# Kernel tuning notes

Hardware: AMD Instinct MI355X
Metric: run time of the kernel (lower is better)

The kernel has to match this reference:

```python
import jax, jax.numpy as jnp
import numpy as np
from itertools import product


def _gen_exps(num_vars, degree):
    return [e for e in product(range(degree + 1), repeat=num_vars) if sum(e) <= degree]

EXP_W = _gen_exps(7, 3)  # 120 terms
EXP_B = _gen_exps(3, 3)  # 20 terms
EXP_M = _gen_exps(5, 3)  # 56 terms (+1 diagonal coeff)


def _powers(x, exps):
    return {e: x ** e for e in exps}


def setup_inputs() -> dict:
    key = jax.random.key(0)
    ks = jax.random.split(key, 12)
    B, Din, Dout = 65536, 64, 64
    return {
        'x1': jax.random.normal(ks[0], (B, Din), jnp.float32),
        's1': jax.random.normal(ks[1], (B, Dout), jnp.float32),
        'y1': jax.random.normal(ks[2], (B, Dout), jnp.float32),
        'x2': jax.random.normal(ks[3], (B, Din), jnp.float32),
        's2': jax.random.normal(ks[4], (B, Dout), jnp.float32),
        'y2': jax.random.normal(ks[5], (B, Dout), jnp.float32),
        'w': jax.random.normal(ks[6], (Dout, Din), jnp.float32) * 0.1,
        'b': jax.random.normal(ks[7], (Dout,), jnp.float32) * 0.1,
        'm': jax.random.normal(ks[8], (Dout, Dout), jnp.float32) * 0.1,
        'params_w': jax.random.normal(ks[9], (len(EXP_W),), jnp.float32) * 0.1,
        'params_b': jax.random.normal(ks[10], (len(EXP_B),), jnp.float32) * 0.1,
        'params_m': jax.random.normal(ks[11], (len(EXP_M) + 1,), jnp.float32) * 0.1,
    }


def _dw(x1, s1, y1, x2, s2, y2, w, params_w):
    px1 = _powers(x1, {e[0] for e in EXP_W})
    ps1 = _powers(s1, {e[1] for e in EXP_W})
    py1 = _powers(y1, {e[2] for e in EXP_W})
    px2 = _powers(x2, {e[3] for e in EXP_W})
    ps2 = _powers(s2, {e[4] for e in EXP_W})
    py2 = _powers(y2, {e[5] for e in EXP_W})
    pw = _powers(w, {e[6] for e in EXP_W})
    inv_b = 1.0 / x1.shape[0]
    delta_w = jnp.zeros_like(w)
    for i, e in enumerate(EXP_W):
        y_term = ps1[e[1]] * py1[e[2]] * ps2[e[4]] * py2[e[5]]  # [B, Dout]
        x_term = px1[e[0]] * px2[e[3]]                          # [B, Din]
        delta_w = delta_w + (params_w[i] * inv_b) * (y_term.T @ x_term) * pw[e[6]]
    return delta_w  # bound=None (identity), l2_reg=0


def _db(y1, y2, b, params_b):
    py1 = _powers(y1, {e[0] for e in EXP_B})
    py2 = _powers(y2, {e[1] for e in EXP_B})
    pb = _powers(b, {e[2] for e in EXP_B})
    inv_b = 1.0 / y1.shape[0]
    delta_b = jnp.zeros_like(b)
    for i, e in enumerate(EXP_B):
        delta_b = delta_b + (params_b[i] * inv_b) * jnp.sum(py1[e[0]] * py2[e[1]], axis=0) * pb[e[2]]
    return delta_b


def _dm(y1, y2, m, params_m):
    ey1 = {e[0] for e in EXP_M} | {e[1] for e in EXP_M}
    ey2 = {e[2] for e in EXP_M} | {e[3] for e in EXP_M}
    py1 = _powers(y1, ey1)
    py2 = _powers(y2, ey2)
    pm = _powers(m, {e[4] for e in EXP_M})
    inv_b = 1.0 / y1.shape[0]
    delta_m = jnp.zeros_like(m)
    for i, e in enumerate(EXP_M):
        left = py1[e[1]] * py2[e[3]]   # [B, Dout]
        right = py1[e[0]] * py2[e[2]]  # [B, Dout]
        delta_m = delta_m + (params_m[i] * inv_b) * (left.T @ right) * pm[e[4]]
    delta_m = delta_m + params_m[-1] * jnp.eye(m.shape[0], dtype=m.dtype)
    return delta_m


def reference(x1, s1, y1, x2, s2, y2, w, b, m, params_w, params_b, params_m):
    delta_w = _dw(x1, s1, y1, x2, s2, y2, w, params_w)
    delta_b = _db(y1, y2, b, params_b)
    delta_m = _dm(y1, y2, m, params_m)
    return delta_w, delta_b, delta_m
```

## Files before the change

kernel.cpp:

```cpp
#include <hip/hip_runtime.h>
#include <type_traits>
#include <stdint.h>

#define DEV __device__ __forceinline__

typedef float f32x4 __attribute__((ext_vector_type(4)));
typedef short bf16x8 __attribute__((ext_vector_type(8)));
typedef unsigned short u16;
typedef u16 u16x8 __attribute__((ext_vector_type(8)));

static constexpr int BTOT = 65536;
static constexpr int KB   = 64;
static constexpr int NCHT = BTOT / KB;
static constexpr int NG   = 56;
static constexpr int NCOLSUM = 45;
static constexpr float INVB = 1.0f / (float)BTOT;

static constexpr int NWIN  = 32;
static constexpr int CHW   = NCHT / NWIN;
static constexpr int NCOLG = 7;
static constexpr int GRID  = 8*NWIN;
static constexpr int BUFHALF = 8*4096;

struct Col {
  int nslot, np;
  int8_t sexp[8][6];
  int8_t pa[8], pb[8];
  int16_t gout[8];
  uint8_t ldmask;
};

struct Tables {
  int nW, nB, nM, nA, nX;
  int8_t expw[120][7];
  int8_t expb[20][3];
  int8_t expm[56][5];
  int8_t am[35][4];
  int8_t xm[10][2];
  Col col[NCOLG];
  int8_t wtype[120]; int16_t widx[120]; int8_t wpow[120];
  int8_t mtype[56];  int16_t midx[56];  int8_t mpow[56];
  int16_t bcol[20];  int8_t bpow[20];
  int err, gcount;
};

constexpr int aidf(const Tables& t,int a,int b,int c,int d){
  for(int i=0;i<t.nA;i++)
    if(t.am[i][0]==a&&t.am[i][1]==b&&t.am[i][2]==c&&t.am[i][3]==d) return i;
  return -1;
}
constexpr int xidf(const Tables& t,int a,int b){
  for(int i=0;i<t.nX;i++) if(t.xm[i][0]==a&&t.xm[i][1]==b) return i;
  return -1;
}

constexpr Tables makeTables(){
  Tables t{};
  t.err = 0;
  t.nW=0;
  for(int e0=0;e0<4;e0++)for(int e1=0;e1<4;e1++)for(int e2=0;e2<4;e2++)
  for(int e3=0;e3<4;e3++)for(int e4=0;e4<4;e4++)for(int e5=0;e5<4;e5++)
  for(int e6=0;e6<4;e6++) if(e0+e1+e2+e3+e4+e5+e6<=3){
    t.expw[t.nW][0]=(int8_t)e0; t.expw[t.nW][1]=(int8_t)e1; t.expw[t.nW][2]=(int8_t)e2;
    t.expw[t.nW][3]=(int8_t)e3; t.expw[t.nW][4]=(int8_t)e4; t.expw[t.nW][5]=(int8_t)e5;
    t.expw[t.nW][6]=(int8_t)e6; t.nW++;
  }
  t.nB=0;
  for(int e0=0;e0<4;e0++)for(int e1=0;e1<4;e1++)for(int e2=0;e2<4;e2++)
    if(e0+e1+e2<=3){ t.expb[t.nB][0]=(int8_t)e0; t.expb[t.nB][1]=(int8_t)e1; t.expb[t.nB][2]=(int8_t)e2; t.nB++; }
  t.nM=0;
  for(int e0=0;e0<4;e0++)for(int e1=0;e1<4;e1++)for(int e2=0;e2<4;e2++)
  for(int e3=0;e3<4;e3++)for(int e4=0;e4<4;e4++)
    if(e0+e1+e2+e3+e4<=3){
      t.expm[t.nM][0]=(int8_t)e0; t.expm[t.nM][1]=(int8_t)e1; t.expm[t.nM][2]=(int8_t)e2;
      t.expm[t.nM][3]=(int8_t)e3; t.expm[t.nM][4]=(int8_t)e4; t.nM++;
    }
  t.nA=0;
  for(int a=0;a<4;a++)for(int b=0;b<4;b++)for(int c=0;c<4;c++)for(int d=0;d<4;d++)
    if(a+b+c+d<=3){ t.am[t.nA][0]=(int8_t)a; t.am[t.nA][1]=(int8_t)b; t.am[t.nA][2]=(int8_t)c; t.am[t.nA][3]=(int8_t)d; t.nA++; }
  t.nX=0;
  for(int a=0;a<4;a++)for(int b=0;b<4;b++)
    if(a+b<=3){ t.xm[t.nX][0]=(int8_t)a; t.xm[t.nX][1]=(int8_t)b; t.nX++; }

  int wslot[35][10]; int mslot[10][10];
  for(int i=0;i<35;i++)for(int j=0;j<10;j++) wslot[i][j]=-1;
  for(int i=0;i<10;i++)for(int j=0;j<10;j++) mslot[i][j]=-1;

  int slot=0;

  {
    Col& c=t.col[0]; c.nslot=4; c.np=8;
    int ym[4][2]={{0,1},{1,0},{0,2},{1,1}};
    for(int s=0;s<4;s++){ for(int q=0;q<6;q++)c.sexp[s][q]=0;
      c.sexp[s][1]=(int8_t)ym[s][0]; c.sexp[s][3]=(int8_t)ym[s][1]; }
    int p=0;
    for(int L=0;L<2;L++)for(int R=0;R<4;R++){
      c.pa[p]=(int8_t)L; c.pb[p]=(int8_t)R; c.gout[p]=(int16_t)slot;
      mslot[xidf(t,ym[L][0],ym[L][1])][xidf(t,ym[R][0],ym[R][1])]=slot; slot++; p++;
    }
  }
  {
    Col& c=t.col[1]; c.nslot=5; c.np=8;
    int ym[5][2]={{0,1},{1,0},{0,2},{1,1},{2,0}};
    for(int s=0;s<5;s++){ for(int q=0;q<6;q++)c.sexp[s][q]=0;
      c.sexp[s][1]=(int8_t)ym[s][0]; c.sexp[s][3]=(int8_t)ym[s][1]; }
    int p=0;
    for(int L=0;L<2;L++){
      c.pa[p]=(int8_t)L; c.pb[p]=4; c.gout[p]=(int16_t)slot;
      mslot[xidf(t,ym[L][0],ym[L][1])][xidf(t,2,0)]=slot; slot++; p++;
    }
    for(int i=0;i<3;i++)for(int j=0;j<2;j++){
      c.pa[p]=(int8_t)(2+i); c.pb[p]=(int8_t)j; c.gout[p]=(int16_t)slot;
      mslot[xidf(t,ym[2+i][0],ym[2+i][1])][xidf(t,ym[j][0],ym[j][1])]=slot; slot++; p++;
    }
  }
  for(int wc=0; wc<2; wc++){
    Col& c=t.col[2+2*wc]; c.nslot=6; c.np=8;
    int am2[2][2]={{1,0},{0,1}};
    int xb[4][2]={{0,1},{1,0},{0,2},{1,1}};
    for(int s=0;s<6;s++) for(int q=0;q<6;q++) c.sexp[s][q]=0;
    for(int s=0;s<2;s++){
      c.sexp[s][wc?2:0]=(int8_t)am2[s][0]; c.sexp[s][wc?3:1]=(int8_t)am2[s][1];
    }
    for(int s=0;s<4;s++){ c.sexp[2+s][4]=(int8_t)xb[s][0]; c.sexp[2+s][5]=(int8_t)xb[s][1]; }
    int p=0;
    for(int a=0;a<2;a++)for(int b=0;b<4;b++){
      int amid = wc? aidf(t,0,0,am2[a][0],am2[a][1]) : aidf(t,am2[a][0],am2[a][1],0,0);
      if(amid<0) t.err+=1;
      c.pa[p]=(int8_t)a; c.pb[p]=(int8_t)(2+b); c.gout[p]=(int16_t)slot;
      wslot[amid][xidf(t,xb[b][0],xb[b][1])]=slot; slot++; p++;
    }
  }
  for(int wc=0; wc<2; wc++){
    Col& c=t.col[3+2*wc]; c.nslot=8; c.np=8;
    int am5[5][2]={{1,0},{0,1},{2,0},{1,1},{0,2}};
    int xb[3][2]={{2,0},{0,1},{1,0}};
    for(int s=0;s<8;s++) for(int q=0;q<6;q++) c.sexp[s][q]=0;
    for(int s=0;s<5;s++){
      c.sexp[s][wc?2:0]=(int8_t)am5[s][0]; c.sexp[s][wc?3:1]=(int8_t)am5[s][1];
    }
    for(int s=0;s<3;s++){ c.sexp[5+s][4]=(int8_t)xb[s][0]; c.sexp[5+s][5]=(int8_t)xb[s][1]; }
    int p=0;
    for(int a=0;a<2;a++){
      int amid = wc? aidf(t,0,0,am5[a][0],am5[a][1]) : aidf(t,am5[a][0],am5[a][1],0,0);
      if(amid<0) t.err+=1;
      c.pa[p]=(int8_t)a; c.pb[p]=5; c.gout[p]=(int16_t)slot;
      wslot[amid][xidf(t,2,0)]=slot; slot++; p++;
    }
    for(int i=0;i<3;i++)for(int j=0;j<2;j++){
      int amid = wc? aidf(t,0,0,am5[2+i][0],am5[2+i][1]) : aidf(t,am5[2+i][0],am5[2+i][1],0,0);
      if(amid<0) t.err+=1;
      c.pa[p]=(int8_t)(2+i); c.pb[p]=(int8_t)(6+j); c.gout[p]=(int16_t)slot;
      wslot[amid][xidf(t,xb[1+j][0],xb[1+j][1])]=slot; slot++; p++;
    }
  }
  {
    Col& c=t.col[6]; c.nslot=6; c.np=8;
    int a4[4][4]={{1,0,1,0},{1,0,0,1},{0,1,1,0},{0,1,0,1}};
    int xb[2][2]={{0,1},{1,0}};
    for(int s=0;s<6;s++) for(int q=0;q<6;q++) c.sexp[s][q]=0;
    for(int s=0;s<4;s++) for(int q=0;q<4;q++) c.sexp[s][q]=(int8_t)a4[s][q];
    for(int s=0;s<2;s++){ c.sexp[4+s][4]=(int8_t)xb[s][0]; c.sexp[4+s][5]=(int8_t)xb[s][1]; }
    int p=0;
    for(int a=0;a<4;a++)for(int b=0;b<2;b++){
      int amid = aidf(t,a4[a][0],a4[a][1],a4[a][2],a4[a][3]);
      if(amid<0) t.err+=1;
      c.pa[p]=(int8_t)a; c.pb[p]=(int8_t)(4+b); c.gout[p]=(int16_t)slot;
      wslot[amid][xidf(t,xb[b][0],xb[b][1])]=slot; slot++; p++;
    }
  }
  t.gcount=slot;
  if(slot!=NG) t.err+=1;

  for(int ci=0; ci<NCOLG; ci++){
    unsigned m=0;
    for(int s=0;s<t.col[ci].nslot;s++)
      for(int v=0;v<6;v++) if(t.col[ci].sexp[s][v]>0) m |= (1u<<v);
    t.col[ci].ldmask=(uint8_t)m;
  }

  for(int i=0;i<t.nW;i++){
    const int8_t* e=t.expw[i];
    bool u0=(e[0]==0&&e[3]==0);
    bool v0=(e[1]==0&&e[2]==0&&e[4]==0&&e[5]==0);
    t.wpow[i]=e[6];
    if(u0){ t.wtype[i]=1; t.widx[i]=(int16_t)aidf(t,e[1],e[2],e[4],e[5]); }
    else if(v0){ t.wtype[i]=2; t.widx[i]=(int16_t)xidf(t,e[0],e[3]); }
    else {
      int s=wslot[aidf(t,e[1],e[2],e[4],e[5])][xidf(t,e[0],e[3])];
      if(s<0) t.err+=1;
      t.wtype[i]=0; t.widx[i]=(int16_t)s;
    }
  }
  for(int i=0;i<t.nM;i++){
    const int8_t* e=t.expm[i];
    bool L0=(e[1]==0&&e[3]==0), R0=(e[0]==0&&e[2]==0);
    t.mpow[i]=e[4];
    if(L0){ t.mtype[i]=2; t.midx[i]=(int16_t)aidf(t,0,e[0],0,e[2]); }
    else if(R0){ t.mtype[i]=1; t.midx[i]=(int16_t)aidf(t,0,e[1],0,e[3]); }
    else {
      int s=mslot[xidf(t,e[1],e[3])][xidf(t,e[0],e[2])];
      if(s<0) t.err+=1;
      t.mtype[i]=0; t.midx[i]=(int16_t)s;
    }
  }
  for(int i=0;i<t.nB;i++){
    const int8_t* e=t.expb[i];
    t.bcol[i]=(int16_t)aidf(t,0,e[0],0,e[1]); t.bpow[i]=e[2];
  }
  return t;
}

constexpr Tables TB = makeTables();
static_assert(TB.err==0 && TB.gcount==56, "table build failed");
static_assert(TB.nW==120 && TB.nB==20 && TB.nM==56 && TB.nA==35 && TB.nX==10, "enumeration mismatch");

template<int N, typename F>
DEV void sunroll(F&& f){
  if constexpr (N > 0){
    sunroll<N-1>(static_cast<F&&>(f));
    f(std::integral_constant<int, N-1>{});
  }
}
template<int E> DEV float ipw(float x){
  if constexpr(E==0) return 1.0f;
  else if constexpr(E==1) return x;
  else if constexpr(E==2) return x*x;
  else return x*x*x;
}
DEV u16 f2bf(float f){
  uint32_t u = __builtin_bit_cast(uint32_t, f);
  u = u + 0x7FFFu + ((u>>16)&1u);
  return (u16)(u>>16);
}

DEV bf16x8 readFrag(const u16* L, int slot, int sb, int tt, int l){
  return *(const bf16x8*)&L[slot*4096 + ((sb*4 + tt)*64 + l)*8];
}
DEV f32x4 mfma_(bf16x8 a, bf16x8 b, f32x4 c){
  return __builtin_amdgcn_mfma_f32_16x16x32_bf16(a, b, c, 0, 0, 0);
}

template<int CI>
DEV void colGemm(const float* __restrict__ s1,const float* __restrict__ y1,
                 const float* __restrict__ s2,const float* __restrict__ y2,
                 const float* __restrict__ x1,const float* __restrict__ x2,
                 float* __restrict__ G, u16* lds, int tid, int bi)
{
  constexpr int NS = TB.col[CI].nslot;
  constexpr unsigned LM = TB.col[CI].ldmask;

  const int l = tid&63, w = tid>>6;
  const int c0 = bi*CHW, c1 = c0+CHW;

  if (w < 8){
    const int pw = w;
    const int wrbase = ((pw>>2)*4 + (l>>4))*512 + ((pw&3)*16 + (l&15))*8;
    float rw[6][8];

    auto LOAD = [&](int ck){
      const int b0 = (ck*KB + pw*8)*64 + l;
      #pragma unroll
      for(int j=0;j<8;j++){
        const int off = b0 + j*64;
        if constexpr(LM&1u)  rw[0][j]=s1[off];
        if constexpr(LM&2u)  rw[1][j]=y1[off];
        if constexpr(LM&4u)  rw[2][j]=s2[off];
        if constexpr(LM&8u)  rw[3][j]=y2[off];
        if constexpr(LM&16u) rw[4][j]=x1[off];
        if constexpr(LM&32u) rw[5][j]=x2[off];
      }
    };
    auto PROD = [&](int buf){
      u16* L = lds + buf*BUFHALF;
      sunroll<NS>([&](auto S){
        constexpr int s = decltype(S)::value;
        u16x8 o8;
        #pragma unroll
        for(int j=0;j<8;j++){
          float v = ipw<TB.col[CI].sexp[s][0]>(rw[0][j])
                  * ipw<TB.col[CI].sexp[s][1]>(rw[1][j])
                  * ipw<TB.col[CI].sexp[s][2]>(rw[2][j])
                  * ipw<TB.col[CI].sexp[s][3]>(rw[3][j])
                  * ipw<TB.col[CI].sexp[s][4]>(rw[4][j])
                  * ipw<TB.col[CI].sexp[s][5]>(rw[5][j]);
          o8[j]=f2bf(v);
        }
        *(u16x8*)&L[s*4096 + wrbase] = o8;
      });
    };

    LOAD(c0); PROD(c0&1);
    asm volatile("s_waitcnt lgkmcnt(0)" ::: "memory");
    __builtin_amdgcn_s_barrier();
    __builtin_amdgcn_sched_barrier(0);

    for(int k=c0; k<c1; ++k){
      if(k+1 < c1){ LOAD(k+1); PROD((k+1)&1); }
      asm volatile("s_waitcnt lgkmcnt(0)" ::: "memory");
      __builtin_amdgcn_s_barrier();
      __builtin_amdgcn_sched_barrier(0);
    }
  } else {
    int aslot=0, bslot=0, gsl=0;
    sunroll<8>([&](auto PP){
      constexpr int p = decltype(PP)::value;
      if(w == 8+p){
        aslot = TB.col[CI].pa[p];
        bslot = TB.col[CI].pb[p];
        gsl   = TB.col[CI].gout[p];
      }
    });
    f32x4 acc[4][4] = {};

    __builtin_amdgcn_s_barrier();
    __builtin_amdgcn_sched_barrier(0);

    for(int k=c0; k<c1; ++k){
      const u16* L = lds + (k&1)*BUFHALF;
      __builtin_amdgcn_s_setprio(1);
      #pragma unroll
      for(int sb=0; sb<2; ++sb){
        bf16x8 Af[4];
        #pragma unroll
        for(int o2=0;o2<4;o2++) Af[o2]=readFrag(L,aslot,sb,o2,l);
        #pragma unroll
        for(int dd=0;dd<4;dd++){
          bf16x8 Bf=readFrag(L,bslot,sb,dd,l);
          #pragma unroll
          for(int o2=0;o2<4;o2++) acc[o2][dd]=mfma_(Af[o2],Bf,acc[o2][dd]);
        }
      }
      __builtin_amdgcn_s_setprio(0);
      asm volatile("s_waitcnt lgkmcnt(0)" ::: "memory");
      __builtin_amdgcn_s_barrier();
      __builtin_amdgcn_sched_barrier(0);
    }

    const int r0=(l>>4)*4, cc=l&15;
    float* dst = G + gsl*4096;
    #pragma unroll
    for(int o2=0;o2<4;o2++)
      #pragma unroll
      for(int dd=0;dd<4;dd++)
        #pragma unroll
        for(int r=0;r<4;r++)
          atomicAdd(&dst[(o2*16+r0+r)*64 + dd*16+cc], acc[o2][dd][r]);
  }
}

DEV void colRed(const float* __restrict__ s1,const float* __restrict__ y1,
                const float* __restrict__ s2,const float* __restrict__ y2,
                const float* __restrict__ x1,const float* __restrict__ x2,
                float* __restrict__ col, float* ldsF, int tid, int bi)
{
  const int ch=tid&63, g16=tid>>6;
  const int base = bi*2048;
  float accv[45];
  sunroll<45>([&](auto K){ accv[decltype(K)::value]=0.f; });
  for(int r=base+g16; r<base+2048; r+=16){
    const int off=r*64+ch;
    const float v0=s1[off],v1=y1[off],v2=s2[off],v3=y2[off],v4=x1[off],v5=x2[off];
    sunroll<35>([&](auto K){
      constexpr int k=decltype(K)::value;
      accv[k] += ipw<TB.am[k][0]>(v0)*ipw<TB.am[k][1]>(v1)*ipw<TB.am[k][2]>(v2)*ipw<TB.am[k][3]>(v3);
    });
    sunroll<10>([&](auto K){
      constexpr int k=decltype(K)::value;
      accv[35+k] += ipw<TB.xm[k][0]>(v4)*ipw<TB.xm[k][1]>(v5);
    });
  }
  sunroll<6>([&](auto RR){
    constexpr int rr=decltype(RR)::value;
    __syncthreads();
    sunroll<8>([&](auto Q){
      constexpr int q=decltype(Q)::value;
      if constexpr(rr*8+q < 45)
        ldsF[(q*16+g16)*64+ch]=accv[rr*8+q];
    });
    __syncthreads();
    {
      const int k=tid>>6, c=tid&63;
      const int idx=rr*8+k;
      if(k<8 && idx<45){
        float s=0.f;
        #pragma unroll
        for(int gg=0; gg<16; gg++) s+=ldsF[(k*16+gg)*64+c];
        atomicAdd(&col[idx*64+c], s);
      }
    }
  });
}

__global__ __launch_bounds__(1024, 4) void k_main(
    const float* __restrict__ x1, const float* __restrict__ s1, const float* __restrict__ y1,
    const float* __restrict__ x2, const float* __restrict__ s2, const float* __restrict__ y2,
    float* __restrict__ G, float* __restrict__ col)
{
  __shared__ u16 lds[2*BUFHALF];
  const int tid = threadIdx.x;
  const int u = blockIdx.x >> 5;
  const int g = blockIdx.x & 31;
  if      (u==0) colGemm<0>(s1,y1,s2,y2,x1,x2,G,lds,tid,g);
  else if (u==1) colGemm<1>(s1,y1,s2,y2,x1,x2,G,lds,tid,g);
  else if (u==2) colGemm<2>(s1,y1,s2,y2,x1,x2,G,lds,tid,g);
  else if (u==3) colGemm<3>(s1,y1,s2,y2,x1,x2,G,lds,tid,g);
  else if (u==4) colGemm<4>(s1,y1,s2,y2,x1,x2,G,lds,tid,g);
  else if (u==5) colGemm<5>(s1,y1,s2,y2,x1,x2,G,lds,tid,g);
  else if (u==6) colGemm<6>(s1,y1,s2,y2,x1,x2,G,lds,tid,g);
  else           colRed(s1,y1,s2,y2,x1,x2,col,(float*)lds,tid,g);
}

__global__ __launch_bounds__(256) void k_combine(
    const float* __restrict__ G, const float* __restrict__ col,
    const float* __restrict__ w, const float* __restrict__ b, const float* __restrict__ m,
    const float* __restrict__ parw, const float* __restrict__ parb, const float* __restrict__ parm,
    float* __restrict__ out)
{
  const int n = blockIdx.x*256 + threadIdx.x;
  const int o = n>>6, d = n&63;
  const float wv = w[n], mv = m[n];
  const float wp[4] = {1.f, wv, wv*wv, wv*wv*wv};
  const float mp[4] = {1.f, mv, mv*mv, mv*mv*mv};
  float aw=0.f, am=0.f;
  sunroll<120>([&](auto II){
    constexpr int i = decltype(II)::value;
    constexpr int ty = TB.wtype[i];
    constexpr int ix = TB.widx[i];
    constexpr int q  = TB.wpow[i];
    float val;
    if constexpr(ty==0) val = G[ix*4096 + n];
    else if constexpr(ty==1) val = col[ix*64 + o];
    else val = col[(35+ix)*64 + d];
    aw += parw[i] * val * wp[q];
  });
  sunroll<56>([&](auto II){
    constexpr int i = decltype(II)::value;
    constexpr int ty = TB.mtype[i];
    constexpr int ix = TB.midx[i];
    constexpr int q  = TB.mpow[i];
    float val;
    if constexpr(ty==0) val = G[ix*4096 + n];
    else if constexpr(ty==1) val = col[ix*64 + o];
    else val = col[ix*64 + d];
    am += parm[i] * val * mp[q];
  });
  aw *= INVB; am *= INVB;
  if (o==d) am += parm[56];
  out[n] = aw;
  out[4160 + n] = am;
  if (n < 64){
    const float bv = b[n];
    const float bp[4] = {1.f, bv, bv*bv, bv*bv*bv};
    float ab=0.f;
    sunroll<20>([&](auto II){
      constexpr int i = decltype(II)::value;
      constexpr int cix = TB.bcol[i];
      constexpr int q = TB.bpow[i];
      ab += parb[i] * col[cix*64 + n] * bp[q];
    });
    out[4096 + n] = ab * INVB;
  }
}

extern "C" void kernel_launch(void* const* d_in, const int* in_sizes, int n_in,
                              void* d_out, int out_size, void* d_ws, size_t ws_size,
                              hipStream_t stream)
{
  const float* x1=(const float*)d_in[0];
  const float* s1=(const float*)d_in[1];
  const float* y1=(const float*)d_in[2];
  const float* x2=(const float*)d_in[3];
  const float* s2=(const float*)d_in[4];
  const float* y2=(const float*)d_in[5];
  const float* w =(const float*)d_in[6];
  const float* b =(const float*)d_in[7];
  const float* m =(const float*)d_in[8];
  const float* parw=(const float*)d_in[9];
  const float* parb=(const float*)d_in[10];
  const float* parm=(const float*)d_in[11];

  float* G   = (float*)d_ws;
  float* col = G + NG*4096;

  hipMemsetAsync(d_ws, 0, (size_t)(NG*4096 + NCOLSUM*64)*sizeof(float), stream);
  k_main<<<GRID, 1024, 0, stream>>>(x1,s1,y1,x2,s2,y2,G,col);
  k_combine<<<16, 256, 0, stream>>>(G,col,w,b,m,parw,parb,parm,(float*)d_out);
}
```

Measured before the change: 107.7 us.

## Fuse column-sum reductions into GEMM producer warps and drop separate reduction blocks

The separate colRed block group, which re-read all six inputs to compute the 45 column sums, is removed. Each column sum is now assigned at compile time to the GEMM column group whose producer warps already load the needed inputs, and is accumulated from the staged registers. The grid shrinks from 8 to 7 block groups, cutting redundant global reads. The change also swaps warp roles (MFMA consumers now in warps 0-7), drops the setprio hint, prefetches input loads one chunk further ahead, and relaxes the launch-bounds occupancy hint, which adds register pressure in the producer warps.

```diff
diff --git a/kernel.cpp b/kernel.cpp
--- a/kernel.cpp
+++ b/kernel.cpp
@@ -19,7 +19,7 @@
 static constexpr int NWIN  = 32;
 static constexpr int CHW   = NCHT / NWIN;
 static constexpr int NCOLG = 7;
-static constexpr int GRID  = 8*NWIN;
+static constexpr int GRID  = NCOLG*NWIN;
 static constexpr int BUFHALF = 8*4096;
 
 struct Col {
@@ -28,6 +28,9 @@
   int8_t pa[8], pb[8];
   int16_t gout[8];
   uint8_t ldmask;
+  int ncs;
+  int8_t csexp[13][6];
+  int8_t csidx[13];
 };
 
 struct Tables {
@@ -41,7 +44,7 @@
   int8_t wtype[120]; int16_t widx[120]; int8_t wpow[120];
   int8_t mtype[56];  int16_t midx[56];  int8_t mpow[56];
   int16_t bcol[20];  int8_t bpow[20];
-  int err, gcount;
+  int err, gcount, cscover;
 };
 
 constexpr int aidf(const Tables& t,int a,int b,int c,int d){
@@ -179,6 +182,34 @@
     t.col[ci].ldmask=(uint8_t)m;
   }
 
+  t.cscover=0;
+  for(int i=0;i<t.nA;i++){
+    const int8_t* e=t.am[i];
+    int target;
+    if(e[0]==0&&e[2]==0) target=0;
+    else if(e[2]==0&&e[3]==0) target=3;
+    else if(e[0]==0&&e[1]==0) target=5;
+    else target=6;
+    Col& c=t.col[target];
+    c.csexp[c.ncs][0]=e[0]; c.csexp[c.ncs][1]=e[1];
+    c.csexp[c.ncs][2]=e[2]; c.csexp[c.ncs][3]=e[3];
+    c.csexp[c.ncs][4]=0; c.csexp[c.ncs][5]=0;
+    c.csidx[c.ncs]=(int8_t)i; c.ncs++; t.cscover++;
+  }
+  for(int i=0;i<t.nX;i++){
+    Col& c=t.col[2];
+    c.csexp[c.ncs][0]=0; c.csexp[c.ncs][1]=0; c.csexp[c.ncs][2]=0; c.csexp[c.ncs][3]=0;
+    c.csexp[c.ncs][4]=t.xm[i][0]; c.csexp[c.ncs][5]=t.xm[i][1];
+    c.csidx[c.ncs]=(int8_t)(35+i); c.ncs++; t.cscover++;
+  }
+  if(t.cscover!=NCOLSUM) t.err+=1;
+  for(int ci=0; ci<NCOLG; ci++){
+    if(t.col[ci].ncs>13) t.err+=1;
+    for(int k=0;k<t.col[ci].ncs;k++)
+      for(int v=0;v<6;v++)
+        if(t.col[ci].csexp[k][v]>0 && !((t.col[ci].ldmask>>v)&1u)) t.err+=1;
+  }
+
   for(int i=0;i<t.nW;i++){
     const int8_t* e=t.expw[i];
     bool u0=(e[0]==0&&e[3]==0);
@@ -212,7 +243,7 @@
 }
 
 constexpr Tables TB = makeTables();
-static_assert(TB.err==0 && TB.gcount==56, "table build failed");
+static_assert(TB.err==0 && TB.gcount==56 && TB.cscover==45, "table build failed");
 static_assert(TB.nW==120 && TB.nB==20 && TB.nM==56 && TB.nA==35 && TB.nX==10, "enumeration mismatch");
 
 template<int N, typename F>
@@ -245,21 +276,68 @@
 DEV void colGemm(const float* __restrict__ s1,const float* __restrict__ y1,
                  const float* __restrict__ s2,const float* __restrict__ y2,
                  const float* __restrict__ x1,const float* __restrict__ x2,
-                 float* __restrict__ G, u16* lds, int tid, int bi)
+                 float* __restrict__ G, float* __restrict__ col,
+                 u16* lds, int tid, int bi)
 {
   constexpr int NS = TB.col[CI].nslot;
+  constexpr int NCS = TB.col[CI].ncs;
   constexpr unsigned LM = TB.col[CI].ldmask;
 
   const int l = tid&63, w = tid>>6;
   const int c0 = bi*CHW, c1 = c0+CHW;
 
   if (w < 8){
-    const int pw = w;
-    const int wrbase = ((pw>>2)*4 + (l>>4))*512 + ((pw&3)*16 + (l&15))*8;
+    int aslot=0, bslot=0, gsl=0;
+    sunroll<8>([&](auto PP){
+      constexpr int p = decltype(PP)::value;
+      if(w == p){
+        aslot = TB.col[CI].pa[p];
+        bslot = TB.col[CI].pb[p];
+        gsl   = TB.col[CI].gout[p];
+      }
+    });
+    f32x4 acc[4][4] = {};
+
+    __builtin_amdgcn_s_barrier();
+    __builtin_amdgcn_sched_barrier(0);
+
+    for(int k=c0; k<c1; ++k){
+      const u16* L = lds + (k&1)*BUFHALF;
+      #pragma unroll
+      for(int sb=0; sb<2; ++sb){
+        bf16x8 Af[4];
+        #pragma unroll
+        for(int o2=0;o2<4;o2++) Af[o2]=readFrag(L,aslot,sb,o2,l);
+        #pragma unroll
+        for(int dd=0;dd<4;dd++){
+          bf16x8 Bf=readFrag(L,bslot,sb,dd,l);
+          #pragma unroll
+          for(int o2=0;o2<4;o2++) acc[o2][dd]=mfma_(Af[o2],Bf,acc[o2][dd]);
+        }
+      }
+      asm volatile("s_waitcnt lgkmcnt(0)" ::: "memory");
+      __builtin_amdgcn_s_barrier();
+      __builtin_amdgcn_sched_barrier(0);
+    }
+
+    const int r0=(l>>4)*4, cc=l&15;
+    float* dst = G + gsl*4096;
+    #pragma unroll
+    for(int o2=0;o2<4;o2++)
+      #pragma unroll
+      for(int dd=0;dd<4;dd++)
+        #pragma unroll
+        for(int r=0;r<4;r++)
+          atomicAdd(&dst[(o2*16+r0+r)*64 + dd*16+cc], acc[o2][dd][r]);
+  } else {
+    const int sw = w-8;
+    const int wrbase = ((sw>>2)*4 + (l>>4))*512 + ((sw&3)*16 + (l&15))*8;
     float rw[6][8];
+    float csum[NCS>0?NCS:1];
+    sunroll<(NCS>0?NCS:1)>([&](auto C){ csum[decltype(C)::value]=0.f; });
 
     auto LOAD = [&](int ck){
-      const int b0 = (ck*KB + pw*8)*64 + l;
+      const int b0 = (ck*KB + sw*8)*64 + l;
       #pragma unroll
       for(int j=0;j<8;j++){
         const int off = b0 + j*64;
@@ -271,7 +349,7 @@
         if constexpr(LM&32u) rw[5][j]=x2[off];
       }
     };
-    auto PROD = [&](int buf){
+    auto STAGE = [&](int buf){
       u16* L = lds + buf*BUFHALF;
       sunroll<NS>([&](auto S){
         constexpr int s = decltype(S)::value;
@@ -289,110 +367,47 @@
         *(u16x8*)&L[s*4096 + wrbase] = o8;
       });
     };
-
-    LOAD(c0); PROD(c0&1);
+    auto CSUM = [&]{
+      sunroll<NCS>([&](auto C){
+        constexpr int c = decltype(C)::value;
+        float s0 = 0.f;
+        #pragma unroll
+        for(int j=0;j<8;j++){
+          s0 += ipw<TB.col[CI].csexp[c][0]>(rw[0][j])
+              * ipw<TB.col[CI].csexp[c][1]>(rw[1][j])
+              * ipw<TB.col[CI].csexp[c][2]>(rw[2][j])
+              * ipw<TB.col[CI].csexp[c][3]>(rw[3][j])
+              * ipw<TB.col[CI].csexp[c][4]>(rw[4][j])
+              * ipw<TB.col[CI].csexp[c][5]>(rw[5][j]);
+        }
+        csum[c] += s0;
+      });
+    };
+
+    LOAD(c0); STAGE(c0&1); CSUM(); LOAD(c0+1);
     asm volatile("s_waitcnt lgkmcnt(0)" ::: "memory");
     __builtin_amdgcn_s_barrier();
     __builtin_amdgcn_sched_barrier(0);
 
     for(int k=c0; k<c1; ++k){
-      if(k+1 < c1){ LOAD(k+1); PROD((k+1)&1); }
+      if(k+1 < c1){
+        STAGE((k+1)&1);
+        CSUM();
+        if(k+2 < c1) LOAD(k+2);
+      }
       asm volatile("s_waitcnt lgkmcnt(0)" ::: "memory");
       __builtin_amdgcn_s_barrier();
       __builtin_amdgcn_sched_barrier(0);
     }
-  } else {
-    int aslot=0, bslot=0, gsl=0;
-    sunroll<8>([&](auto PP){
-      constexpr int p = decltype(PP)::value;
-      if(w == 8+p){
-        aslot = TB.col[CI].pa[p];
-        bslot = TB.col[CI].pb[p];
-        gsl   = TB.col[CI].gout[p];
-      }
+
+    sunroll<NCS>([&](auto C){
+      constexpr int c = decltype(C)::value;
+      atomicAdd(&col[(int)TB.col[CI].csidx[c]*64 + l], csum[c]);
     });
-    f32x4 acc[4][4] = {};
-
-    __builtin_amdgcn_s_barrier();
-    __builtin_amdgcn_sched_barrier(0);
-
-    for(int k=c0; k<c1; ++k){
-      const u16* L = lds + (k&1)*BUFHALF;
-      __builtin_amdgcn_s_setprio(1);
-      #pragma unroll
-      for(int sb=0; sb<2; ++sb){
-        bf16x8 Af[4];
-        #pragma unroll
-        for(int o2=0;o2<4;o2++) Af[o2]=readFrag(L,aslot,sb,o2,l);
-        #pragma unroll
-        for(int dd=0;dd<4;dd++){
-          bf16x8 Bf=readFrag(L,bslot,sb,dd,l);
-          #pragma unroll
-          for(int o2=0;o2<4;o2++) acc[o2][dd]=mfma_(Af[o2],Bf,acc[o2][dd]);
-        }
-      }
-      __builtin_amdgcn_s_setprio(0);
-      asm volatile("s_waitcnt lgkmcnt(0)" ::: "memory");
-      __builtin_amdgcn_s_barrier();
-      __builtin_amdgcn_sched_barrier(0);
-    }
-
-    const int r0=(l>>4)*4, cc=l&15;
-    float* dst = G + gsl*4096;
-    #pragma unroll
-    for(int o2=0;o2<4;o2++)
-      #pragma unroll
-      for(int dd=0;dd<4;dd++)
-        #pragma unroll
-        for(int r=0;r<4;r++)
-          atomicAdd(&dst[(o2*16+r0+r)*64 + dd*16+cc], acc[o2][dd][r]);
-  }
-}
-
-DEV void colRed(const float* __restrict__ s1,const float* __restrict__ y1,
-                const float* __restrict__ s2,const float* __restrict__ y2,
-                const float* __restrict__ x1,const float* __restrict__ x2,
-                float* __restrict__ col, float* ldsF, int tid, int bi)
-{
-  const int ch=tid&63, g16=tid>>6;
-  const int base = bi*2048;
-  float accv[45];
-  sunroll<45>([&](auto K){ accv[decltype(K)::value]=0.f; });
-  for(int r=base+g16; r<base+2048; r+=16){
-    const int off=r*64+ch;
-    const float v0=s1[off],v1=y1[off],v2=s2[off],v3=y2[off],v4=x1[off],v5=x2[off];
-    sunroll<35>([&](auto K){
-      constexpr int k=decltype(K)::value;
-      accv[k] += ipw<TB.am[k][0]>(v0)*ipw<TB.am[k][1]>(v1)*ipw<TB.am[k][2]>(v2)*ipw<TB.am[k][3]>(v3);
-    });
-    sunroll<10>([&](auto K){
-      constexpr int k=decltype(K)::value;
-      accv[35+k] += ipw<TB.xm[k][0]>(v4)*ipw<TB.xm[k][1]>(v5);
-    });
-  }
-  sunroll<6>([&](auto RR){
-    constexpr int rr=decltype(RR)::value;
-    __syncthreads();
-    sunroll<8>([&](auto Q){
-      constexpr int q=decltype(Q)::value;
-      if constexpr(rr*8+q < 45)
-        ldsF[(q*16+g16)*64+ch]=accv[rr*8+q];
-    });
-    __syncthreads();
-    {
-      const int k=tid>>6, c=tid&63;
-      const int idx=rr*8+k;
-      if(k<8 && idx<45){
-        float s=0.f;
-        #pragma unroll
-        for(int gg=0; gg<16; gg++) s+=ldsF[(k*16+gg)*64+c];
-        atomicAdd(&col[idx*64+c], s);
-      }
-    }
-  });
-}
-
-__global__ __launch_bounds__(1024, 4) void k_main(
+  }
+}
+
+__global__ __launch_bounds__(1024) void k_main(
     const float* __restrict__ x1, const float* __restrict__ s1, const float* __restrict__ y1,
     const float* __restrict__ x2, const float* __restrict__ s2, const float* __restrict__ y2,
     float* __restrict__ G, float* __restrict__ col)
@@ -401,14 +416,13 @@
   const int tid = threadIdx.x;
   const int u = blockIdx.x >> 5;
   const int g = blockIdx.x & 31;
-  if      (u==0) colGemm<0>(s1,y1,s2,y2,x1,x2,G,lds,tid,g);
-  else if (u==1) colGemm<1>(s1,y1,s2,y2,x1,x2,G,lds,tid,g);
-  else if (u==2) colGemm<2>(s1,y1,s2,y2,x1,x2,G,lds,tid,g);
-  else if (u==3) colGemm<3>(s1,y1,s2,y2,x1,x2,G,lds,tid,g);
-  else if (u==4) colGemm<4>(s1,y1,s2,y2,x1,x2,G,lds,tid,g);
-  else if (u==5) colGemm<5>(s1,y1,s2,y2,x1,x2,G,lds,tid,g);
-  else if (u==6) colGemm<6>(s1,y1,s2,y2,x1,x2,G,lds,tid,g);
-  else           colRed(s1,y1,s2,y2,x1,x2,col,(float*)lds,tid,g);
+  if      (u==0) colGemm<0>(s1,y1,s2,y2,x1,x2,G,col,lds,tid,g);
+  else if (u==1) colGemm<1>(s1,y1,s2,y2,x1,x2,G,col,lds,tid,g);
+  else if (u==2) colGemm<2>(s1,y1,s2,y2,x1,x2,G,col,lds,tid,g);
+  else if (u==3) colGemm<3>(s1,y1,s2,y2,x1,x2,G,col,lds,tid,g);
+  else if (u==4) colGemm<4>(s1,y1,s2,y2,x1,x2,G,col,lds,tid,g);
+  else if (u==5) colGemm<5>(s1,y1,s2,y2,x1,x2,G,col,lds,tid,g);
+  else           colGemm<6>(s1,y1,s2,y2,x1,x2,G,col,lds,tid,g);
 }
 
 __global__ __launch_bounds__(256) void k_combine(
```

Result: slower. 280.4 us (+160.3%).

## Merge producer and MFMA waves into unified 512-thread blocks with more windows

Applied to the files above, without the earlier changes.

Drops warp specialization, in which 8 waves produced bf16 power products into a double-buffered LDS and 8 other waves ran MFMAs. Now every wave of a 512-thread block computes its own products, writes them to a single LDS buffer, then runs its GEMM slot pair, with two barriers per chunk. The grid doubles to 64 windows per column group, and the column-reduction blocks are adjusted to 8 row groups. This halves LDS use and may let more blocks fit per CU, at the cost of losing the overlap between product computation and MFMA within a block and doubling the atomic adds to G.

```diff
diff --git a/kernel.cpp b/kernel.cpp
--- a/kernel.cpp
+++ b/kernel.cpp
@@ -16,11 +16,10 @@
 static constexpr int NCOLSUM = 45;
 static constexpr float INVB = 1.0f / (float)BTOT;
 
-static constexpr int NWIN  = 32;
+static constexpr int NWIN  = 64;
 static constexpr int CHW   = NCHT / NWIN;
 static constexpr int NCOLG = 7;
 static constexpr int GRID  = 8*NWIN;
-static constexpr int BUFHALF = 8*4096;
 
 struct Col {
   int nslot, np;
@@ -251,102 +250,81 @@
   constexpr unsigned LM = TB.col[CI].ldmask;
 
   const int l = tid&63, w = tid>>6;
+  const int wrbase = ((w>>2)*4 + (l>>4))*512 + ((w&3)*16 + (l&15))*8;
+
+  int aslot=0, bslot=0, gsl=0;
+  sunroll<8>([&](auto PP){
+    constexpr int p = decltype(PP)::value;
+    if(w == p){
+      aslot = TB.col[CI].pa[p];
+      bslot = TB.col[CI].pb[p];
+      gsl   = TB.col[CI].gout[p];
+    }
+  });
+
   const int c0 = bi*CHW, c1 = c0+CHW;
-
-  if (w < 8){
-    const int pw = w;
-    const int wrbase = ((pw>>2)*4 + (l>>4))*512 + ((pw&3)*16 + (l&15))*8;
-    float rw[6][8];
-
-    auto LOAD = [&](int ck){
-      const int b0 = (ck*KB + pw*8)*64 + l;
-      #pragma unroll
-      for(int j=0;j<8;j++){
-        const int off = b0 + j*64;
-        if constexpr(LM&1u)  rw[0][j]=s1[off];
-        if constexpr(LM&2u)  rw[1][j]=y1[off];
-        if constexpr(LM&4u)  rw[2][j]=s2[off];
-        if constexpr(LM&8u)  rw[3][j]=y2[off];
-        if constexpr(LM&16u) rw[4][j]=x1[off];
-        if constexpr(LM&32u) rw[5][j]=x2[off];
-      }
-    };
-    auto PROD = [&](int buf){
-      u16* L = lds + buf*BUFHALF;
+  f32x4 acc[4][4] = {};
+
+  for(int k=c0; k<c1; ++k){
+    u16x8 o8v[NS];
+    const int b0 = (k*KB + w*8)*64 + l;
+    #pragma unroll
+    for(int j=0;j<8;j++){
+      const int off = b0 + j*64;
+      float v0=0,v1=0,v2=0,v3=0,v4=0,v5=0;
+      if constexpr(LM&1u)  v0=s1[off];
+      if constexpr(LM&2u)  v1=y1[off];
+      if constexpr(LM&4u)  v2=s2[off];
+      if constexpr(LM&8u)  v3=y2[off];
+      if constexpr(LM&16u) v4=x1[off];
+      if constexpr(LM&32u) v5=x2[off];
       sunroll<NS>([&](auto S){
         constexpr int s = decltype(S)::value;
-        u16x8 o8;
-        #pragma unroll
-        for(int j=0;j<8;j++){
-          float v = ipw<TB.col[CI].sexp[s][0]>(rw[0][j])
-                  * ipw<TB.col[CI].sexp[s][1]>(rw[1][j])
-                  * ipw<TB.col[CI].sexp[s][2]>(rw[2][j])
-                  * ipw<TB.col[CI].sexp[s][3]>(rw[3][j])
-                  * ipw<TB.col[CI].sexp[s][4]>(rw[4][j])
-                  * ipw<TB.col[CI].sexp[s][5]>(rw[5][j]);
-          o8[j]=f2bf(v);
-        }
-        *(u16x8*)&L[s*4096 + wrbase] = o8;
+        float v = ipw<TB.col[CI].sexp[s][0]>(v0)
+                * ipw<TB.col[CI].sexp[s][1]>(v1)
+                * ipw<TB.col[CI].sexp[s][2]>(v2)
+                * ipw<TB.col[CI].sexp[s][3]>(v3)
+                * ipw<TB.col[CI].sexp[s][4]>(v4)
+                * ipw<TB.col[CI].sexp[s][5]>(v5);
+        o8v[s][j] = f2bf(v);
       });
-    };
-
-    LOAD(c0); PROD(c0&1);
+    }
+    sunroll<NS>([&](auto S){
+      constexpr int s = decltype(S)::value;
+      *(u16x8*)&lds[s*4096 + wrbase] = o8v[s];
+    });
+
     asm volatile("s_waitcnt lgkmcnt(0)" ::: "memory");
     __builtin_amdgcn_s_barrier();
     __builtin_amdgcn_sched_barrier(0);
 
-    for(int k=c0; k<c1; ++k){
-      if(k+1 < c1){ LOAD(k+1); PROD((k+1)&1); }
-      asm volatile("s_waitcnt lgkmcnt(0)" ::: "memory");
-      __builtin_amdgcn_s_barrier();
-      __builtin_amdgcn_sched_barrier(0);
-    }
-  } else {
-    int aslot=0, bslot=0, gsl=0;
-    sunroll<8>([&](auto PP){
-      constexpr int p = decltype(PP)::value;
-      if(w == 8+p){
-        aslot = TB.col[CI].pa[p];
-        bslot = TB.col[CI].pb[p];
-        gsl   = TB.col[CI].gout[p];
+    #pragma unroll
+    for(int sb=0; sb<2; ++sb){
+      bf16x8 Af[4];
+      #pragma unroll
+      for(int o2=0;o2<4;o2++) Af[o2]=readFrag(lds,aslot,sb,o2,l);
+      #pragma unroll
+      for(int dd=0;dd<4;dd++){
+        bf16x8 Bf=readFrag(lds,bslot,sb,dd,l);
+        #pragma unroll
+        for(int o2=0;o2<4;o2++) acc[o2][dd]=mfma_(Af[o2],Bf,acc[o2][dd]);
       }
-    });
-    f32x4 acc[4][4] = {};
-
+    }
+
+    asm volatile("s_waitcnt lgkmcnt(0)" ::: "memory");
     __builtin_amdgcn_s_barrier();
     __builtin_amdgcn_sched_barrier(0);
-
-    for(int k=c0; k<c1; ++k){
-      const u16* L = lds + (k&1)*BUFHALF;
-      __builtin_amdgcn_s_setprio(1);
+  }
+
+  const int r0=(l>>4)*4, cc=l&15;
+  float* dst = G + gsl*4096;
+  #pragma unroll
+  for(int o2=0;o2<4;o2++)
+    #pragma unroll
+    for(int dd=0;dd<4;dd++)
       #pragma unroll
-      for(int sb=0; sb<2; ++sb){
-        bf16x8 Af[4];
-        #pragma unroll
-        for(int o2=0;o2<4;o2++) Af[o2]=readFrag(L,aslot,sb,o2,l);
-        #pragma unroll
-        for(int dd=0;dd<4;dd++){
-          bf16x8 Bf=readFrag(L,bslot,sb,dd,l);
-          #pragma unroll
-          for(int o2=0;o2<4;o2++) acc[o2][dd]=mfma_(Af[o2],Bf,acc[o2][dd]);
-        }
-      }
-      __builtin_amdgcn_s_setprio(0);
-      asm volatile("s_waitcnt lgkmcnt(0)" ::: "memory");
-      __builtin_amdgcn_s_barrier();
-      __builtin_amdgcn_sched_barrier(0);
-    }
-
-    const int r0=(l>>4)*4, cc=l&15;
-    float* dst = G + gsl*4096;
-    #pragma unroll
-    for(int o2=0;o2<4;o2++)
-      #pragma unroll
-      for(int dd=0;dd<4;dd++)
-        #pragma unroll
-        for(int r=0;r<4;r++)
-          atomicAdd(&dst[(o2*16+r0+r)*64 + dd*16+cc], acc[o2][dd][r]);
-  }
+      for(int r=0;r<4;r++)
+        atomicAdd(&dst[(o2*16+r0+r)*64 + dd*16+cc], acc[o2][dd][r]);
 }
 
 DEV void colRed(const float* __restrict__ s1,const float* __restrict__ y1,
@@ -354,11 +332,11 @@
                 const float* __restrict__ x1,const float* __restrict__ x2,
                 float* __restrict__ col, float* ldsF, int tid, int bi)
 {
-  const int ch=tid&63, g16=tid>>6;
-  const int base = bi*2048;
+  const int ch=tid&63, g8=tid>>6;
+  const int base = bi*1024;
   float accv[45];
   sunroll<45>([&](auto K){ accv[decltype(K)::value]=0.f; });
-  for(int r=base+g16; r<base+2048; r+=16){
+  for(int r=base+g8; r<base+1024; r+=8){
     const int off=r*64+ch;
     const float v0=s1[off],v1=y1[off],v2=s2[off],v3=y2[off],v4=x1[off],v5=x2[off];
     sunroll<35>([&](auto K){
@@ -376,31 +354,31 @@
     sunroll<8>([&](auto Q){
       constexpr int q=decltype(Q)::value;
       if constexpr(rr*8+q < 45)
-        ldsF[(q*16+g16)*64+ch]=accv[rr*8+q];
+        ldsF[(q*8+g8)*64+ch]=accv[rr*8+q];
     });
     __syncthreads();
     {
       const int k=tid>>6, c=tid&63;
       const int idx=rr*8+k;
-      if(k<8 && idx<45){
+      if(idx<45){
         float s=0.f;
         #pragma unroll
-        for(int gg=0; gg<16; gg++) s+=ldsF[(k*16+gg)*64+c];
+        for(int gg=0; gg<8; gg++) s+=ldsF[(k*8+gg)*64+c];
         atomicAdd(&col[idx*64+c], s);
       }
     }
   });
 }
 
-__global__ __launch_bounds__(1024, 4) void k_main(
+__global__ __launch_bounds__(512, 4) void k_main(
     const float* __restrict__ x1, const float* __restrict__ s1, const float* __restrict__ y1,
     const float* __restrict__ x2, const float* __restrict__ s2, const float* __restrict__ y2,
     float* __restrict__ G, float* __restrict__ col)
 {
-  __shared__ u16 lds[2*BUFHALF];
+  __shared__ u16 lds[8*4096];
   const int tid = threadIdx.x;
-  const int u = blockIdx.x >> 5;
-  const int g = blockIdx.x & 31;
+  const int u = blockIdx.x >> 6;
+  const int g = blockIdx.x & 63;
   if      (u==0) colGemm<0>(s1,y1,s2,y2,x1,x2,G,lds,tid,g);
   else if (u==1) colGemm<1>(s1,y1,s2,y2,x1,x2,G,lds,tid,g);
   else if (u==2) colGemm<2>(s1,y1,s2,y2,x1,x2,G,lds,tid,g);
@@ -484,6 +462,6 @@
   float* col = G + NG*4096;
 
   hipMemsetAsync(d_ws, 0, (size_t)(NG*4096 + NCOLSUM*64)*sizeof(float), stream);
-  k_main<<<GRID, 1024, 0, stream>>>(x1,s1,y1,x2,s2,y2,G,col);
+  k_main<<<GRID, 512, 0, stream>>>(x1,s1,y1,x2,s2,y2,G,col);
   k_combine<<<16, 256, 0, stream>>>(G,col,w,b,m,parw,parb,parm,(float*)d_out);
 }
```

Result: slower. 118.7 us (+10.2%).
